# Kernel optimization log

Hardware: AMD Instinct MI355X
Metric: run time of the kernel (lower is better)

## Reference

```python
import jax, jax.numpy as jnp
import numpy as np

N, S, D, E, L = 16, 2048, 256, 512, 4
SEP_P = 1.0 / 48.0  # separator probability -> ~40 ragged subsequences per row


def _ends_per_row(m):
    # Mirrors torch subseqs_from_mask: yields (i, j) for nonempty runs between
    # True separators; we record the LAST index (j-1) of each run.
    ends = []
    i = 0
    Slen = len(m)
    for t in range(Slen):
        if m[t]:
            if i != t:
                ends.append(t - 1)
            i = t + 1
    if i != Slen:
        ends.append(Slen - 1)
    return ends


def _mask_np():
    rng = np.random.default_rng(0)
    return rng.random((N, S)) < SEP_P


def _gather_indices(mask_np):
    ends = [_ends_per_row(row) for row in mask_np]
    Sp = max(max((len(e) for e in ends), default=1), 1)
    idx = np.zeros((len(ends), Sp), dtype=np.int64)
    valid = np.zeros((len(ends), Sp), dtype=bool)
    for i, e in enumerate(ends):
        idx[i, : len(e)] = e
        valid[i, : len(e)] = True
    return idx, valid


def setup_inputs() -> dict:
    key = jax.random.key(0)
    ks = jax.random.split(key, 6)
    k = 1.0 / np.sqrt(E)  # torch LSTM default init scale
    u = lambda kk, shape: jax.random.uniform(kk, shape, jnp.float32, -k, k)
    return {
        "pre_embedding": jax.random.normal(ks[0], (N, S, D), jnp.float32),
        "preembed_mask": jnp.asarray(_mask_np()),
        "W_ih0": u(ks[1], (4 * E, D)),
        "W_ih_rest": u(ks[2], (L - 1, 4 * E, E)),
        "W_hh": u(ks[3], (L, 4 * E, E)),
        "b_ih": u(ks[4], (L, 4 * E)),
        "b_hh": u(ks[5], (L, 4 * E)),
    }


def _lstm_scan(x, sep, W_ih0, W_ih_rest, W_hh, b_ih, b_hh):
    # Fused ragged LSTM: one batched scan over time, resetting (h, c) to zero
    # immediately after separator positions. This reproduces running a fresh
    # LSTM on every mask-delimited subsequence (as the torch loop does).
    # x: (N,S,D), sep: (N,S) bool -> ys: (N,S,E) top-layer outputs.
    n = x.shape[0]
    h0 = jnp.zeros((L, n, E), x.dtype)
    c0 = jnp.zeros((L, n, E), x.dtype)

    def step(carry, inputs):
        h, c = carry
        xt, st = inputs  # (N,D), (N,)
        inp = xt
        hs, cs = [], []
        for l in range(L):
            Wi = W_ih0 if l == 0 else W_ih_rest[l - 1]
            gates = inp @ Wi.T + b_ih[l] + h[l] @ W_hh[l].T + b_hh[l]  # (N,4E)
            gi, gf, gg, go = jnp.split(gates, 4, axis=-1)  # torch gate order i,f,g,o
            cl = jax.nn.sigmoid(gf) * c[l] + jax.nn.sigmoid(gi) * jnp.tanh(gg)
            hl = jax.nn.sigmoid(go) * jnp.tanh(cl)
            hs.append(hl)
            cs.append(cl)
            inp = hl
        h_new = jnp.stack(hs)
        c_new = jnp.stack(cs)
        y = h_new[-1]  # (N,E) top layer output at this step
        reset = st[None, :, None]
        return (jnp.where(reset, 0.0, h_new), jnp.where(reset, 0.0, c_new)), y

    (_, _), ys = jax.lax.scan(step, (h0, c0), (x.transpose(1, 0, 2), sep.T))
    return ys.transpose(1, 0, 2)  # (N,S,E)


def reference(pre_embedding, preembed_mask, W_ih0, W_ih_rest, W_hh, b_ih, b_hh):
    n, s = pre_embedding.shape[:2]
    x = pre_embedding.reshape(n, s, -1)  # Flatten(start_dim=2)
    mask_np = np.asarray(preembed_mask)
    idx, valid = _gather_indices(mask_np)  # (N,Sp) host-side, static structure
    ys = _lstm_scan(x, preembed_mask, W_ih0, W_ih_rest, W_hh, b_ih, b_hh)
    rows = jnp.arange(n)[:, None]
    gathered = ys[rows, jnp.asarray(idx)]  # (N,Sp,E) last output of each subsequence
    valid_j = jnp.asarray(valid)
    ret = jnp.where(valid_j[..., None], gathered, 0.0)  # zero padding as in torch
    out_mask = ~valid_j  # torch returns mask==True for padded slots
    return ret, out_mask
```

## Files before the change

### kernel.cpp

```cpp
#include <hip/hip_runtime.h>
#include <hip/hip_bf16.h>

#define NB 16
#define SB 2048
#define DB 256
#define EB 512
#define LB 4
#define NPAR 4
#define NSEG_CAP 1024
#define GRID_MAIN 128

typedef __bf16 bf16x8 __attribute__((ext_vector_type(8)));
typedef float  f32x4  __attribute__((ext_vector_type(4)));
typedef float  f32x16 __attribute__((ext_vector_type(16)));

#define OFF_XBF   0ull
#define SZ_XBF    (16ull*2048*256*2)
#define OFF_W     (OFF_XBF + SZ_XBF)
#define SZ_W      (4ull*2048*1024*2)
#define OFF_BIAS  (OFF_W + SZ_W)
#define OFF_H     (OFF_BIAS + 4ull*2048*4)
#define SZ_H      (4ull*NPAR*NSEG_CAP*EB*2)
#define OFF_C     (OFF_H + SZ_H)
#define SZ_C      (4ull*NSEG_CAP*EB*4)
#define OFF_SROW   (OFF_C + SZ_C)
#define OFF_SSTART (OFF_SROW  + 4ull*NSEG_CAP)
#define OFF_SLEN   (OFF_SSTART + 4ull*NSEG_CAP)
#define OFF_SSLOT  (OFF_SLEN  + 4ull*NSEG_CAP)
#define OFF_ACT   (OFF_SSLOT + 4ull*NSEG_CAP)
#define OFF_META  (OFF_ACT + 4ull*2048)
#define OFF_FLAGS (OFF_META + 256ull)
#define SZ_FLAGS  (4ull*2048*32*4)

__device__ __forceinline__ unsigned short f2bf(float f) {
  union { float f; unsigned u; } v; v.f = f;
  unsigned r = v.u + 0x7FFFu + ((v.u >> 16) & 1u);
  return (unsigned short)(r >> 16);
}
__device__ __forceinline__ float sigf(float x) {
  x = fminf(30.f, fmaxf(-30.f, x));
  return 1.f / (1.f + __expf(-x));
}
__device__ __forceinline__ float tanhx(float x) {
  x = fminf(15.f, fmaxf(-15.f, x));
  float e = __expf(-2.f * x);
  return (1.f - e) / (1.f + e);
}

__global__ void k_conv(const float* __restrict__ x, const float* __restrict__ wih0,
                       const float* __restrict__ wihr, const float* __restrict__ whh,
                       const float* __restrict__ bih, const float* __restrict__ bhh,
                       float* __restrict__ dout, int out_size, char* __restrict__ ws) {
  long long gid = (long long)blockIdx.x * blockDim.x + threadIdx.x;
  long long stride = (long long)gridDim.x * blockDim.x;
  for (long long i = gid; i < out_size; i += stride) dout[i] = 0.f;
  unsigned* hz = (unsigned*)(ws + OFF_H);
  long long hcw = (long long)(SZ_H + SZ_C) / 4;
  for (long long i = gid; i < hcw; i += stride) hz[i] = 0u;
  unsigned* fz = (unsigned*)(ws + OFF_FLAGS);
  for (long long i = gid; i < (long long)(SZ_FLAGS / 4); i += stride) fz[i] = 0u;
  float* bias = (float*)(ws + OFF_BIAS);
  for (long long i = gid; i < 4 * 2048; i += stride) bias[i] = bih[i] + bhh[i];
  unsigned short* wbf = (unsigned short*)(ws + OFF_W);
  for (long long i = gid; i < 4ll * 2048 * 1024; i += stride) {
    int l = (int)(i >> 21);
    int rem = (int)(i & ((1 << 21) - 1));
    int n = rem >> 10, k = rem & 1023;
    float v;
    if (l == 0)
      v = (k < 256) ? wih0[n * 256 + k]
        : (k < 512) ? 0.f
        : whh[(long long)n * 512 + (k - 512)];
    else
      v = (k < 512) ? wihr[((long long)(l - 1) * 2048 + n) * 512 + k]
                    : whh[((long long)l * 2048 + n) * 512 + (k - 512)];
    wbf[i] = f2bf(v);
  }
  unsigned short* xb = (unsigned short*)(ws + OFF_XBF);
  for (long long i = gid; i < (long long)NB * SB * DB; i += stride) xb[i] = f2bf(x[i]);
}

__global__ void k_seg(const void* __restrict__ maskp, char* __restrict__ ws,
                      float* __restrict__ dout, int Sp) {
  __shared__ unsigned bits[NB][64];
  __shared__ int hist[2050];
  __shared__ int sufx[2051];
  __shared__ int part[256];
  __shared__ unsigned metapk[NSEG_CAP];
  __shared__ int slotar[NSEG_CAP];
  __shared__ int rowcnt[NB];
  __shared__ int flagbits, nseg, maxlen;
  int tid = threadIdx.x;
  if (tid == 0) { flagbits = 0; nseg = 0; maxlen = 0; }
  for (int i = tid; i < 2050; i += 256) hist[i] = 0;
  __syncthreads();
  const unsigned* mw = (const unsigned*)maskp;
  int fb = 0;
  for (int i = tid; i < 8192; i += 256) {
    unsigned w = mw[i];
    if (w == 0x3F800000u) fb |= 2;
    if (w == 0x3FF00000u) fb |= 4;
    if (w & 0xFFFFFF00u) fb |= 1;
    if ((i & 1) && w) fb |= 8;
  }
  if (fb) atomicOr(&flagbits, fb);
  __syncthreads();
  int f = flagbits;
  int kind = (f & 4) ? 3 : (f & 2) ? 2 : (f & 1) ? 0 : (f & 8) ? 1 : 3;
  for (int w = tid; w < NB * 64; w += 256) {
    int row = w >> 6, j = w & 63;
    unsigned b = 0;
    int t0 = j * 32;
    for (int z = 0; z < 32; ++z) {
      long long idx = (long long)row * SB + t0 + z;
      bool sep;
      if (kind == 0)      sep = ((const unsigned char*)maskp)[idx] != 0;
      else if (kind == 1) sep = ((const int*)maskp)[idx] != 0;
      else if (kind == 2) sep = ((const float*)maskp)[idx] != 0.f;
      else                sep = ((const unsigned long long*)maskp)[idx] != 0ull;
      b |= (sep ? 1u : 0u) << z;
    }
    bits[row][j] = b;
  }
  __syncthreads();
  if (tid < NB) {
    int row = tid, i = 0, cnt = 0;
    for (int w = 0; w < 64; ++w) {
      unsigned b = bits[row][w];
      while (b) {
        int z = __ffs(b) - 1; b &= b - 1;
        int t = w * 32 + z;
        if (i != t) {
          int len = t - i;
          int idx = atomicAdd(&nseg, 1);
          if (idx < NSEG_CAP) { metapk[idx] = ((unsigned)row << 23) | ((unsigned)i << 12) | (unsigned)len; slotar[idx] = cnt; }
          atomicAdd(&hist[len], 1); atomicMax(&maxlen, len);
          cnt++;
        }
        i = t + 1;
      }
    }
    if (i != SB) {
      int len = SB - i;
      int idx = atomicAdd(&nseg, 1);
      if (idx < NSEG_CAP) { metapk[idx] = ((unsigned)row << 23) | ((unsigned)i << 12) | (unsigned)len; slotar[idx] = cnt; }
      atomicAdd(&hist[len], 1); atomicMax(&maxlen, len);
      cnt++;
    }
    rowcnt[row] = cnt;
  }
  __syncthreads();
  {
    int lo = tid * 9, hi = lo + 9; if (hi > 2050) hi = 2050;
    int s = 0;
    for (int k = lo; k < hi; ++k) s += hist[k];
    part[tid] = s;
  }
  __syncthreads();
  {
    int tail = 0;
    for (int t2 = tid + 1; t2 < 256; ++t2) tail += part[t2];
    int lo = tid * 9, hi = lo + 9; if (hi > 2050) hi = 2050;
    int run = tail;
    for (int k = hi - 1; k >= lo; --k) { run += hist[k]; sufx[k] = run; }
  }
  __syncthreads();
  int* act = (int*)(ws + OFF_ACT);
  for (int r = tid; r < 2048; r += 256) act[r] = sufx[r + 1];
  for (int i = tid; i < 2050; i += 256) hist[i] = 0;
  __syncthreads();
  int NSEG = nseg < NSEG_CAP ? nseg : NSEG_CAP;
  int* srow = (int*)(ws + OFF_SROW);
  int* sstart = (int*)(ws + OFF_SSTART);
  int* slen = (int*)(ws + OFF_SLEN);
  int* sslot = (int*)(ws + OFF_SSLOT);
  for (int i = tid; i < NSEG; i += 256) {
    unsigned m = metapk[i];
    int len = m & 0xFFF, st = (m >> 12) & 0x7FF, row = (int)(m >> 23);
    int pos = sufx[len + 1] + atomicAdd(&hist[len], 1);
    srow[pos] = row; sstart[pos] = st; slen[pos] = len; sslot[pos] = slotar[i];
  }
  int* meta = (int*)(ws + OFF_META);
  if (tid == 0) { meta[0] = NSEG; meta[1] = maxlen; }
  __syncthreads();
  float* omask = dout + (long long)NB * Sp * EB;
  for (int i = tid; i < NB * Sp; i += 256) {
    int row = i / Sp, slot = i % Sp;
    omask[i] = (slot < rowcnt[row]) ? 0.f : 1.f;
  }
}

__global__ void __launch_bounds__(512, 2)
k_main(char* __restrict__ ws, float* __restrict__ dout, int Sp) {
  __shared__ float glds[2][64][65];
  __shared__ float bias_s[64];
  __shared__ int act_s[2048];
  const int tid = threadIdx.x;
  const int l = blockIdx.x >> 5, wb = blockIdx.x & 31, e0 = wb << 4;
  const int wave = tid >> 6, lane = tid & 63;
  const int mh = wave & 1, kh = (wave >> 1) & 1, rg = wave >> 2;
  const int l31 = lane & 31, lhi = lane >> 5;

  {
    const int* act = (const int*)(ws + OFF_ACT);
    for (int i = tid; i < 2048; i += 512) act_s[i] = act[i];
    if (tid < 64) bias_s[tid] =
        ((const float*)(ws + OFF_BIAS))[l * 2048 + (tid >> 4) * 512 + e0 + (tid & 15)];
  }
  const int maxlen = ((const int*)(ws + OFF_META))[1];
  const char* wsb = ws;

  bf16x8 breg[32];
  {
    int rho = rg * 32 + l31;
    int g = rho >> 4, e = rho & 15;
    const char* wrow = wsb + OFF_W + ((size_t)(l * 2048 + g * 512 + e0 + e)) * 2048;
    const int kbase = kh * 512 + lhi * 8;
    #pragma unroll
    for (int t = 0; t < 32; ++t)
      breg[t] = *(const bf16x8*)(wrow + (size_t)(kbase + t * 16) * 2);
  }
  __syncthreads();

  const int* srow  = (const int*)(ws + OFF_SROW);
  const int* sstart = (const int*)(ws + OFF_SSTART);
  const int* slen  = (const int*)(ws + OFF_SLEN);
  const int* sslot = (const int*)(ws + OFF_SSLOT);
  unsigned* flags = (unsigned*)(ws + OFF_FLAGS);
  const bool l0k0 = (l == 0) && (kh == 0);

  for (int r = 0; r < maxlen; ++r) {
    const bool nA = (l > 0), nB = (r > 0), nC = (l < 3) && (r >= 4);
    if (wave == 0 && (nA | nB | nC)) {
      int li = lane & 31;
      while (true) {
        unsigned ok = 1;
        if (nA) ok &= (__hip_atomic_load(flags + ((((l - 1) * 2048 + r) << 5) + li),
                                         __ATOMIC_RELAXED, __HIP_MEMORY_SCOPE_AGENT) != 0);
        if (nB) ok &= (__hip_atomic_load(flags + (((l * 2048 + (r - 1)) << 5) + li),
                                         __ATOMIC_RELAXED, __HIP_MEMORY_SCOPE_AGENT) != 0);
        if (nC) ok &= (__hip_atomic_load(flags + ((((l + 1) * 2048 + (r - 4)) << 5) + li),
                                         __ATOMIC_RELAXED, __HIP_MEMORY_SCOPE_AGENT) != 0);
        if (__all((int)ok)) break;
        __builtin_amdgcn_s_sleep(2);
      }
      __threadfence();
    }
    __syncthreads();

    const int M = act_s[r];
    const int nmch = (M + 63) >> 6;
    for (int mch = 0; mch < nmch; ++mch) {
      const int segbase = mch << 6;
      int Mv = M - segbase; if (Mv > 64) Mv = 64;
      const int m_l = mh * 32 + l31;
      const int sg = segbase + ((m_l < Mv) ? m_l : 0);
      const char* abase;
      if (kh == 0) {
        if (l == 0) {
          int rw = srow[sg], st = sstart[sg];
          abase = wsb + OFF_XBF + ((size_t)((rw * SB + st + r)) * DB + lhi * 8) * 2;
        } else {
          abase = wsb + OFF_H + ((size_t)((((l - 1) * NPAR + (r & 3)) * NSEG_CAP) + sg) * EB + lhi * 8) * 2;
        }
      } else {
        abase = wsb + OFF_H + ((size_t)(((l * NPAR + ((r - 1) & 3)) * NSEG_CAP) + sg) * EB + lhi * 8) * 2;
      }
      f32x16 acc0 = {0.f}, acc1 = {0.f};
      #pragma unroll
      for (int i = 0; i < 16; ++i) { acc0[i] = 0.f; acc1[i] = 0.f; }
      #pragma unroll
      for (int t = 0; t < 16; t += 2) {
        bf16x8 a0 = *(const bf16x8*)(abase + t * 32);
        acc0 = __builtin_amdgcn_mfma_f32_32x32x16_bf16(a0, breg[t], acc0, 0, 0, 0);
        bf16x8 a1 = *(const bf16x8*)(abase + (t + 1) * 32);
        acc1 = __builtin_amdgcn_mfma_f32_32x32x16_bf16(a1, breg[t + 1], acc1, 0, 0, 0);
      }
      if (!l0k0) {
        #pragma unroll
        for (int t = 16; t < 32; t += 2) {
          bf16x8 a0 = *(const bf16x8*)(abase + t * 32);
          acc0 = __builtin_amdgcn_mfma_f32_32x32x16_bf16(a0, breg[t], acc0, 0, 0, 0);
          bf16x8 a1 = *(const bf16x8*)(abase + (t + 1) * 32);
          acc1 = __builtin_amdgcn_mfma_f32_32x32x16_bf16(a1, breg[t + 1], acc1, 0, 0, 0);
        }
      }
      #pragma unroll
      for (int reg = 0; reg < 16; ++reg) {
        int mm = mh * 32 + (reg & 3) + 8 * (reg >> 2) + 4 * lhi;
        glds[kh][mm][rg * 32 + l31] = acc0[reg] + acc1[reg];
      }
      __syncthreads();
      #pragma unroll
      for (int q = 0; q < 2; ++q) {
        int cell = tid + (q << 9);
        int e = cell & 15, m = cell >> 4;
        if (m < Mv) {
          int sg2 = segbase + m;
          float gi = glds[0][m][e]      + glds[1][m][e]      + bias_s[e];
          float gf = glds[0][m][16 + e] + glds[1][m][16 + e] + bias_s[16 + e];
          float gg = glds[0][m][32 + e] + glds[1][m][32 + e] + bias_s[32 + e];
          float go = glds[0][m][48 + e] + glds[1][m][48 + e] + bias_s[48 + e];
          float* cptr = (float*)(ws + OFF_C + ((size_t)(l * NSEG_CAP + sg2) * EB + e0 + e) * 4);
          float cold = *cptr;
          float cnew = sigf(gf) * cold + sigf(gi) * tanhx(gg);
          float hnew = sigf(go) * tanhx(cnew);
          *cptr = cnew;
          *(unsigned short*)(ws + OFF_H +
              ((size_t)(((l * NPAR + (r & 3)) * NSEG_CAP) + sg2) * EB + e0 + e) * 2) = f2bf(hnew);
          if (l == 3) {
            if (r == slen[sg2] - 1) {
              int rw = srow[sg2], sl = sslot[sg2];
              if (sl < Sp) dout[(((long long)rw * Sp + sl) << 9) + e0 + e] = hnew;
            }
          }
        }
      }
      __syncthreads();
    }
    if (tid == 0) {
      __threadfence();
      __hip_atomic_store(flags + (((l * 2048 + r) << 5) + wb), 1u,
                         __ATOMIC_RELEASE, __HIP_MEMORY_SCOPE_AGENT);
    }
  }
}

extern "C" void kernel_launch(void* const* d_in, const int* in_sizes, int n_in,
                              void* d_out, int out_size, void* d_ws, size_t ws_size,
                              hipStream_t stream) {
  const float* x    = (const float*)d_in[0];
  const void*  mask = d_in[1];
  const float* wih0 = (const float*)d_in[2];
  const float* wihr = (const float*)d_in[3];
  const float* whh  = (const float*)d_in[4];
  const float* bih  = (const float*)d_in[5];
  const float* bhh  = (const float*)d_in[6];
  float* out = (float*)d_out;
  char* ws = (char*)d_ws;
  int Sp = out_size / (NB * (EB + 1));

  k_conv<<<dim3(2048), dim3(256), 0, stream>>>(x, wih0, wihr, whh, bih, bhh, out, out_size, ws);
  k_seg<<<dim3(1), dim3(256), 0, stream>>>(mask, ws, out, Sp);
  k_main<<<dim3(GRID_MAIN), dim3(512), 0, stream>>>(ws, out, Sp);
}
```

Baseline: 7.540 ms.

## Split persistent LSTM wavefront kernel across 512 blocks with LDS-resident weights

The persistent layer-wavefront kernel now uses 128 blocks per layer, each owning 4 hidden units (16 gate rows), instead of 32 blocks of 16 units. Weights move from 32 VGPR bf16x8 registers per lane into an LDS tile, and the matmul switches from 32x32x16 to 16x16x32 MFMA with the K split across two wave groups. Precomputed x offsets and the c-state and segment metadata are prefetched before the MFMA loop. This spreads the per-timestep GEMV across more CUs and lowers register pressure to allow 4 blocks per CU, at the cost of 4x more flag polling per step and more redundant A-operand (h/x) loads across blocks.

```diff
diff --git a/kernel.cpp b/kernel.cpp
--- a/kernel.cpp
+++ b/kernel.cpp
@@ -8,11 +8,10 @@
 #define LB 4
 #define NPAR 4
 #define NSEG_CAP 1024
-#define GRID_MAIN 128
+#define GRID_MAIN 512
 
 typedef __bf16 bf16x8 __attribute__((ext_vector_type(8)));
 typedef float  f32x4  __attribute__((ext_vector_type(4)));
-typedef float  f32x16 __attribute__((ext_vector_type(16)));
 
 #define OFF_XBF   0ull
 #define SZ_XBF    (16ull*2048*256*2)
@@ -27,10 +26,11 @@
 #define OFF_SSTART (OFF_SROW  + 4ull*NSEG_CAP)
 #define OFF_SLEN   (OFF_SSTART + 4ull*NSEG_CAP)
 #define OFF_SSLOT  (OFF_SLEN  + 4ull*NSEG_CAP)
-#define OFF_ACT   (OFF_SSLOT + 4ull*NSEG_CAP)
+#define OFF_XOFF   (OFF_SSLOT + 4ull*NSEG_CAP)
+#define OFF_ACT   (OFF_XOFF + 4ull*NSEG_CAP)
 #define OFF_META  (OFF_ACT + 4ull*2048)
 #define OFF_FLAGS (OFF_META + 256ull)
-#define SZ_FLAGS  (4ull*2048*32*4)
+#define SZ_FLAGS  (4ull*2048*128*4)
 
 __device__ __forceinline__ unsigned short f2bf(float f) {
   union { float f; unsigned u; } v; v.f = f;
@@ -174,11 +174,13 @@
   int* sstart = (int*)(ws + OFF_SSTART);
   int* slen = (int*)(ws + OFF_SLEN);
   int* sslot = (int*)(ws + OFF_SSLOT);
+  int* xoff = (int*)(ws + OFF_XOFF);
   for (int i = tid; i < NSEG; i += 256) {
     unsigned m = metapk[i];
     int len = m & 0xFFF, st = (m >> 12) & 0x7FF, row = (int)(m >> 23);
     int pos = sufx[len + 1] + atomicAdd(&hist[len], 1);
     srow[pos] = row; sstart[pos] = st; slen[pos] = len; sslot[pos] = slotar[i];
+    xoff[pos] = row * SB + st;
   }
   int* meta = (int*)(ws + OFF_META);
   if (tid == 0) { meta[0] = NSEG; meta[1] = maxlen; }
@@ -190,57 +192,57 @@
   }
 }
 
-__global__ void __launch_bounds__(512, 2)
+__global__ void __launch_bounds__(512, 4)
 k_main(char* __restrict__ ws, float* __restrict__ dout, int Sp) {
-  __shared__ float glds[2][64][65];
-  __shared__ float bias_s[64];
-  __shared__ int act_s[2048];
+  __shared__ __align__(16) __bf16 wlds[128][16][8];
+  __shared__ float glds[2][64][17];
+  __shared__ float bias_s[16];
+  __shared__ short act_s[2048];
+  __shared__ unsigned short xoff_s[NSEG_CAP];
   const int tid = threadIdx.x;
-  const int l = blockIdx.x >> 5, wb = blockIdx.x & 31, e0 = wb << 4;
+  const int l = blockIdx.x >> 7, wb = blockIdx.x & 127, e0 = wb << 2;
   const int wave = tid >> 6, lane = tid & 63;
-  const int mh = wave & 1, kh = (wave >> 1) & 1, rg = wave >> 2;
-  const int l31 = lane & 31, lhi = lane >> 5;
+  const int mf = wave & 3, kq = wave >> 2;
+  const int l15 = lane & 15, lq = lane >> 4;
+  const char* wsb = ws;
 
   {
     const int* act = (const int*)(ws + OFF_ACT);
-    for (int i = tid; i < 2048; i += 512) act_s[i] = act[i];
-    if (tid < 64) bias_s[tid] =
-        ((const float*)(ws + OFF_BIAS))[l * 2048 + (tid >> 4) * 512 + e0 + (tid & 15)];
+    for (int i = tid; i < 2048; i += 512) act_s[i] = (short)act[i];
+    const int* xoff = (const int*)(ws + OFF_XOFF);
+    for (int i = tid; i < NSEG_CAP; i += 512) xoff_s[i] = (unsigned short)xoff[i];
+    if (tid < 16) bias_s[tid] =
+        ((const float*)(ws + OFF_BIAS))[l * 2048 + (tid >> 2) * 512 + e0 + (tid & 3)];
+    int rho = tid & 15, g = rho >> 2, e = rho & 3;
+    const unsigned short* wsrc = (const unsigned short*)(wsb + OFF_W)
+        + ((size_t)(l * 2048 + g * 512 + e0 + e)) * 1024;
+    int kg0 = (tid >> 4) * 4;
+    #pragma unroll
+    for (int j = 0; j < 4; ++j)
+      *(bf16x8*)&wlds[kg0 + j][rho][0] = *(const bf16x8*)(wsrc + (size_t)(kg0 + j) * 8);
   }
   const int maxlen = ((const int*)(ws + OFF_META))[1];
-  const char* wsb = ws;
-
-  bf16x8 breg[32];
-  {
-    int rho = rg * 32 + l31;
-    int g = rho >> 4, e = rho & 15;
-    const char* wrow = wsb + OFF_W + ((size_t)(l * 2048 + g * 512 + e0 + e)) * 2048;
-    const int kbase = kh * 512 + lhi * 8;
-    #pragma unroll
-    for (int t = 0; t < 32; ++t)
-      breg[t] = *(const bf16x8*)(wrow + (size_t)(kbase + t * 16) * 2);
-  }
   __syncthreads();
 
   const int* srow  = (const int*)(ws + OFF_SROW);
-  const int* sstart = (const int*)(ws + OFF_SSTART);
   const int* slen  = (const int*)(ws + OFF_SLEN);
   const int* sslot = (const int*)(ws + OFF_SSLOT);
   unsigned* flags = (unsigned*)(ws + OFF_FLAGS);
-  const bool l0k0 = (l == 0) && (kh == 0);
 
   for (int r = 0; r < maxlen; ++r) {
     const bool nA = (l > 0), nB = (r > 0), nC = (l < 3) && (r >= 4);
     if (wave == 0 && (nA | nB | nC)) {
-      int li = lane & 31;
+      const unsigned* pa = flags + ((((l - 1) * 2048 + r) << 7) + lane);
+      const unsigned* pb = flags + (((l * 2048 + (r - 1)) << 7) + lane);
+      const unsigned* pc = flags + ((((l + 1) * 2048 + (r - 4)) << 7) + lane);
       while (true) {
         unsigned ok = 1;
-        if (nA) ok &= (__hip_atomic_load(flags + ((((l - 1) * 2048 + r) << 5) + li),
-                                         __ATOMIC_RELAXED, __HIP_MEMORY_SCOPE_AGENT) != 0);
-        if (nB) ok &= (__hip_atomic_load(flags + (((l * 2048 + (r - 1)) << 5) + li),
-                                         __ATOMIC_RELAXED, __HIP_MEMORY_SCOPE_AGENT) != 0);
-        if (nC) ok &= (__hip_atomic_load(flags + ((((l + 1) * 2048 + (r - 4)) << 5) + li),
-                                         __ATOMIC_RELAXED, __HIP_MEMORY_SCOPE_AGENT) != 0);
+        if (nA) ok &= (__hip_atomic_load(pa, __ATOMIC_RELAXED, __HIP_MEMORY_SCOPE_AGENT) != 0)
+                    & (__hip_atomic_load(pa + 64, __ATOMIC_RELAXED, __HIP_MEMORY_SCOPE_AGENT) != 0);
+        if (nB) ok &= (__hip_atomic_load(pb, __ATOMIC_RELAXED, __HIP_MEMORY_SCOPE_AGENT) != 0)
+                    & (__hip_atomic_load(pb + 64, __ATOMIC_RELAXED, __HIP_MEMORY_SCOPE_AGENT) != 0);
+        if (nC) ok &= (__hip_atomic_load(pc, __ATOMIC_RELAXED, __HIP_MEMORY_SCOPE_AGENT) != 0)
+                    & (__hip_atomic_load(pc + 64, __ATOMIC_RELAXED, __HIP_MEMORY_SCOPE_AGENT) != 0);
         if (__all((int)ok)) break;
         __builtin_amdgcn_s_sleep(2);
       }
@@ -253,74 +255,59 @@
     for (int mch = 0; mch < nmch; ++mch) {
       const int segbase = mch << 6;
       int Mv = M - segbase; if (Mv > 64) Mv = 64;
-      const int m_l = mh * 32 + l31;
+      const int m_l = (mf << 4) + l15;
       const int sg = segbase + ((m_l < Mv) ? m_l : 0);
-      const char* abase;
-      if (kh == 0) {
+      const char* ap;
+      if (kq == 0) {
         if (l == 0) {
-          int rw = srow[sg], st = sstart[sg];
-          abase = wsb + OFF_XBF + ((size_t)((rw * SB + st + r)) * DB + lhi * 8) * 2;
+          ap = wsb + OFF_XBF + (((size_t)((int)xoff_s[sg] + r)) * DB + lq * 8) * 2;
         } else {
-          abase = wsb + OFF_H + ((size_t)((((l - 1) * NPAR + (r & 3)) * NSEG_CAP) + sg) * EB + lhi * 8) * 2;
+          ap = wsb + OFF_H + ((size_t)((((l - 1) * NPAR + (r & 3)) * NSEG_CAP) + sg) * EB + lq * 8) * 2;
         }
       } else {
-        abase = wsb + OFF_H + ((size_t)(((l * NPAR + ((r - 1) & 3)) * NSEG_CAP) + sg) * EB + lhi * 8) * 2;
-      }
-      f32x16 acc0 = {0.f}, acc1 = {0.f};
+        ap = wsb + OFF_H + ((size_t)(((l * NPAR + ((r - 1) & 3)) * NSEG_CAP) + sg) * EB + lq * 8) * 2;
+      }
+      const int em = tid >> 2, ee = tid & 3;
+      float cold = 0.f; int slenv = 0, srowv = 0, sslotv = 0;
+      float* cptr = (float*)(ws + OFF_C + ((size_t)(l * NSEG_CAP + segbase + em) * EB + e0 + ee) * 4);
+      if (tid < 256) {
+        cold = *cptr;
+        if (l == 3) {
+          int sg2 = segbase + em;
+          slenv = slen[sg2]; srowv = srow[sg2]; sslotv = sslot[sg2];
+        }
+      }
+      f32x4 acc = {0.f, 0.f, 0.f, 0.f};
       #pragma unroll
-      for (int i = 0; i < 16; ++i) { acc0[i] = 0.f; acc1[i] = 0.f; }
+      for (int t = 0; t < 16; ++t) {
+        bf16x8 a = *(const bf16x8*)(ap + t * 64);
+        bf16x8 b = *(const bf16x8*)&wlds[(kq << 6) + (t << 2) + lq][l15][0];
+        acc = __builtin_amdgcn_mfma_f32_16x16x32_bf16(a, b, acc, 0, 0, 0);
+      }
       #pragma unroll
-      for (int t = 0; t < 16; t += 2) {
-        bf16x8 a0 = *(const bf16x8*)(abase + t * 32);
-        acc0 = __builtin_amdgcn_mfma_f32_32x32x16_bf16(a0, breg[t], acc0, 0, 0, 0);
-        bf16x8 a1 = *(const bf16x8*)(abase + (t + 1) * 32);
-        acc1 = __builtin_amdgcn_mfma_f32_32x32x16_bf16(a1, breg[t + 1], acc1, 0, 0, 0);
-      }
-      if (!l0k0) {
-        #pragma unroll
-        for (int t = 16; t < 32; t += 2) {
-          bf16x8 a0 = *(const bf16x8*)(abase + t * 32);
-          acc0 = __builtin_amdgcn_mfma_f32_32x32x16_bf16(a0, breg[t], acc0, 0, 0, 0);
-          bf16x8 a1 = *(const bf16x8*)(abase + (t + 1) * 32);
-          acc1 = __builtin_amdgcn_mfma_f32_32x32x16_bf16(a1, breg[t + 1], acc1, 0, 0, 0);
-        }
-      }
-      #pragma unroll
-      for (int reg = 0; reg < 16; ++reg) {
-        int mm = mh * 32 + (reg & 3) + 8 * (reg >> 2) + 4 * lhi;
-        glds[kh][mm][rg * 32 + l31] = acc0[reg] + acc1[reg];
-      }
+      for (int reg = 0; reg < 4; ++reg)
+        glds[kq][(mf << 4) + (lq << 2) + reg][l15] = acc[reg];
       __syncthreads();
-      #pragma unroll
-      for (int q = 0; q < 2; ++q) {
-        int cell = tid + (q << 9);
-        int e = cell & 15, m = cell >> 4;
-        if (m < Mv) {
-          int sg2 = segbase + m;
-          float gi = glds[0][m][e]      + glds[1][m][e]      + bias_s[e];
-          float gf = glds[0][m][16 + e] + glds[1][m][16 + e] + bias_s[16 + e];
-          float gg = glds[0][m][32 + e] + glds[1][m][32 + e] + bias_s[32 + e];
-          float go = glds[0][m][48 + e] + glds[1][m][48 + e] + bias_s[48 + e];
-          float* cptr = (float*)(ws + OFF_C + ((size_t)(l * NSEG_CAP + sg2) * EB + e0 + e) * 4);
-          float cold = *cptr;
-          float cnew = sigf(gf) * cold + sigf(gi) * tanhx(gg);
-          float hnew = sigf(go) * tanhx(cnew);
-          *cptr = cnew;
-          *(unsigned short*)(ws + OFF_H +
-              ((size_t)(((l * NPAR + (r & 3)) * NSEG_CAP) + sg2) * EB + e0 + e) * 2) = f2bf(hnew);
-          if (l == 3) {
-            if (r == slen[sg2] - 1) {
-              int rw = srow[sg2], sl = sslot[sg2];
-              if (sl < Sp) dout[(((long long)rw * Sp + sl) << 9) + e0 + e] = hnew;
-            }
-          }
+      if (tid < 256 && em < Mv) {
+        int sg2 = segbase + em;
+        float gi = glds[0][em][ee]      + glds[1][em][ee]      + bias_s[ee];
+        float gf = glds[0][em][4 + ee]  + glds[1][em][4 + ee]  + bias_s[4 + ee];
+        float gg = glds[0][em][8 + ee]  + glds[1][em][8 + ee]  + bias_s[8 + ee];
+        float go = glds[0][em][12 + ee] + glds[1][em][12 + ee] + bias_s[12 + ee];
+        float cnew = sigf(gf) * cold + sigf(gi) * tanhx(gg);
+        float hnew = sigf(go) * tanhx(cnew);
+        *cptr = cnew;
+        *(unsigned short*)(ws + OFF_H +
+            ((size_t)(((l * NPAR + (r & 3)) * NSEG_CAP) + sg2) * EB + e0 + ee) * 2) = f2bf(hnew);
+        if (l == 3 && r == slenv - 1) {
+          if (sslotv < Sp) dout[(((long long)srowv * Sp + sslotv) << 9) + e0 + ee] = hnew;
         }
       }
       __syncthreads();
     }
     if (tid == 0) {
       __threadfence();
-      __hip_atomic_store(flags + (((l * 2048 + r) << 5) + wb), 1u,
+      __hip_atomic_store(flags + (((l * 2048 + r) << 7) + wb), 1u,
                          __ATOMIC_RELEASE, __HIP_MEMORY_SCOPE_AGENT);
     }
   }
```

After: 15.19 ms. 102% more time.

## Switch recurrent LSTM step to 16x16x32 MFMA tiling with LDS segment metadata

Applied to the files above, without the earlier changes.

Re-tiles the per-step gate GEMM. Each wave now owns one gate (16 columns) across all 64 segments using 16x16x32 bf16 MFMAs, with the K dimension split across two wave groups, instead of 32x32x16 MFMAs over half the rows. Segment metadata (x offsets, lengths, slots, rows) is cached in LDS, the cell state is preloaded before the MFMA loop, and the two K halves are reduced in a single LDS tile. The aim is to cut weight registers, drop global metadata loads from the inner loop, and overlap the c-state load with compute. The trade-off is an extra LDS reduction phase, occupancy lowered to one block per CU, and a larger flags allocation.

```diff
diff --git a/kernel.cpp b/kernel.cpp
--- a/kernel.cpp
+++ b/kernel.cpp
@@ -12,7 +12,6 @@
 
 typedef __bf16 bf16x8 __attribute__((ext_vector_type(8)));
 typedef float  f32x4  __attribute__((ext_vector_type(4)));
-typedef float  f32x16 __attribute__((ext_vector_type(16)));
 
 #define OFF_XBF   0ull
 #define SZ_XBF    (16ull*2048*256*2)
@@ -27,10 +26,11 @@
 #define OFF_SSTART (OFF_SROW  + 4ull*NSEG_CAP)
 #define OFF_SLEN   (OFF_SSTART + 4ull*NSEG_CAP)
 #define OFF_SSLOT  (OFF_SLEN  + 4ull*NSEG_CAP)
-#define OFF_ACT   (OFF_SSLOT + 4ull*NSEG_CAP)
+#define OFF_XOFF   (OFF_SSLOT + 4ull*NSEG_CAP)
+#define OFF_ACT   (OFF_XOFF + 4ull*NSEG_CAP)
 #define OFF_META  (OFF_ACT + 4ull*2048)
 #define OFF_FLAGS (OFF_META + 256ull)
-#define SZ_FLAGS  (4ull*2048*32*4)
+#define SZ_FLAGS  (4ull*2048*128*4)
 
 __device__ __forceinline__ unsigned short f2bf(float f) {
   union { float f; unsigned u; } v; v.f = f;
@@ -174,11 +174,13 @@
   int* sstart = (int*)(ws + OFF_SSTART);
   int* slen = (int*)(ws + OFF_SLEN);
   int* sslot = (int*)(ws + OFF_SSLOT);
+  int* xoff = (int*)(ws + OFF_XOFF);
   for (int i = tid; i < NSEG; i += 256) {
     unsigned m = metapk[i];
     int len = m & 0xFFF, st = (m >> 12) & 0x7FF, row = (int)(m >> 23);
     int pos = sufx[len + 1] + atomicAdd(&hist[len], 1);
     srow[pos] = row; sstart[pos] = st; slen[pos] = len; sslot[pos] = slotar[i];
+    xoff[pos] = row * SB + st;
   }
   int* meta = (int*)(ws + OFF_META);
   if (tid == 0) { meta[0] = NSEG; meta[1] = maxlen; }
@@ -190,44 +192,47 @@
   }
 }
 
-__global__ void __launch_bounds__(512, 2)
+__global__ void __launch_bounds__(512, 1)
 k_main(char* __restrict__ ws, float* __restrict__ dout, int Sp) {
-  __shared__ float glds[2][64][65];
+  __shared__ float glds[64][68];
+  __shared__ unsigned segpk_s[NSEG_CAP];
+  __shared__ unsigned short xoff_s[NSEG_CAP];
+  __shared__ unsigned short act_s[2048];
   __shared__ float bias_s[64];
-  __shared__ int act_s[2048];
   const int tid = threadIdx.x;
   const int l = blockIdx.x >> 5, wb = blockIdx.x & 31, e0 = wb << 4;
   const int wave = tid >> 6, lane = tid & 63;
-  const int mh = wave & 1, kh = (wave >> 1) & 1, rg = wave >> 2;
-  const int l31 = lane & 31, lhi = lane >> 5;
+  const int nq = wave & 3, kh = wave >> 2;
+  const int l15 = lane & 15, lq = lane >> 4;
+  const char* wsb = ws;
 
   {
     const int* act = (const int*)(ws + OFF_ACT);
-    for (int i = tid; i < 2048; i += 512) act_s[i] = act[i];
+    for (int i = tid; i < 2048; i += 512) act_s[i] = (unsigned short)act[i];
+    const int* xoff = (const int*)(ws + OFF_XOFF);
+    const int* srow = (const int*)(ws + OFF_SROW);
+    const int* slen = (const int*)(ws + OFF_SLEN);
+    const int* sslot = (const int*)(ws + OFF_SSLOT);
+    for (int i = tid; i < NSEG_CAP; i += 512) {
+      xoff_s[i] = (unsigned short)xoff[i];
+      segpk_s[i] = ((unsigned)slen[i] & 0xFFFu) | (((unsigned)sslot[i] & 0xFFFu) << 16)
+                 | (((unsigned)srow[i] & 0xFu) << 28);
+    }
     if (tid < 64) bias_s[tid] =
         ((const float*)(ws + OFF_BIAS))[l * 2048 + (tid >> 4) * 512 + e0 + (tid & 15)];
   }
   const int maxlen = ((const int*)(ws + OFF_META))[1];
-  const char* wsb = ws;
-
-  bf16x8 breg[32];
+
+  bf16x8 breg[16];
   {
-    int rho = rg * 32 + l31;
-    int g = rho >> 4, e = rho & 15;
-    const char* wrow = wsb + OFF_W + ((size_t)(l * 2048 + g * 512 + e0 + e)) * 2048;
-    const int kbase = kh * 512 + lhi * 8;
+    const char* wrow = wsb + OFF_W + ((size_t)(l * 2048 + nq * 512 + e0 + l15)) * 2048;
     #pragma unroll
-    for (int t = 0; t < 32; ++t)
-      breg[t] = *(const bf16x8*)(wrow + (size_t)(kbase + t * 16) * 2);
-  }
-  __syncthreads();
-
-  const int* srow  = (const int*)(ws + OFF_SROW);
-  const int* sstart = (const int*)(ws + OFF_SSTART);
-  const int* slen  = (const int*)(ws + OFF_SLEN);
-  const int* sslot = (const int*)(ws + OFF_SSLOT);
+    for (int t = 0; t < 16; ++t)
+      breg[t] = *(const bf16x8*)(wrow + (size_t)(kh * 512 + t * 32 + lq * 8) * 2);
+  }
+  __syncthreads();
+
   unsigned* flags = (unsigned*)(ws + OFF_FLAGS);
-  const bool l0k0 = (l == 0) && (kh == 0);
 
   for (int r = 0; r < maxlen; ++r) {
     const bool nA = (l > 0), nB = (r > 0), nC = (l < 3) && (r >= 4);
@@ -253,65 +258,74 @@
     for (int mch = 0; mch < nmch; ++mch) {
       const int segbase = mch << 6;
       int Mv = M - segbase; if (Mv > 64) Mv = 64;
-      const int m_l = mh * 32 + l31;
-      const int sg = segbase + ((m_l < Mv) ? m_l : 0);
-      const char* abase;
+      const char* ap[4];
+      #pragma unroll
+      for (int mf = 0; mf < 4; ++mf) {
+        int m_l = (mf << 4) + l15;
+        int sg = segbase + ((m_l < Mv) ? m_l : 0);
+        const char* base;
+        if (kh == 0) {
+          if (l == 0)
+            base = wsb + OFF_XBF + (((size_t)((int)xoff_s[sg] + r)) * DB) * 2;
+          else
+            base = wsb + OFF_H + ((size_t)((((l - 1) * NPAR + (r & 3)) * NSEG_CAP) + sg) * EB) * 2;
+        } else {
+          base = wsb + OFF_H + ((size_t)(((l * NPAR + ((r - 1) & 3)) * NSEG_CAP) + sg) * EB) * 2;
+        }
+        ap[mf] = base + lq * 16;
+      }
+      const int em = tid >> 4, ee = tid & 15;
+      float* cp0 = (float*)(ws + OFF_C + ((size_t)(l * NSEG_CAP + segbase + em) * EB + e0 + ee) * 4);
+      float* cp1 = (float*)(ws + OFF_C + ((size_t)(l * NSEG_CAP + segbase + em + 32) * EB + e0 + ee) * 4);
+      float cold0 = *cp0, cold1 = *cp1;
+      f32x4 acc[4];
+      #pragma unroll
+      for (int mf = 0; mf < 4; ++mf) acc[mf] = (f32x4){0.f, 0.f, 0.f, 0.f};
+      #pragma unroll
+      for (int t = 0; t < 16; ++t) {
+        #pragma unroll
+        for (int mf = 0; mf < 4; ++mf) {
+          bf16x8 a = *(const bf16x8*)(ap[mf] + t * 64);
+          acc[mf] = __builtin_amdgcn_mfma_f32_16x16x32_bf16(a, breg[t], acc[mf], 0, 0, 0);
+        }
+      }
       if (kh == 0) {
-        if (l == 0) {
-          int rw = srow[sg], st = sstart[sg];
-          abase = wsb + OFF_XBF + ((size_t)((rw * SB + st + r)) * DB + lhi * 8) * 2;
-        } else {
-          abase = wsb + OFF_H + ((size_t)((((l - 1) * NPAR + (r & 3)) * NSEG_CAP) + sg) * EB + lhi * 8) * 2;
-        }
-      } else {
-        abase = wsb + OFF_H + ((size_t)(((l * NPAR + ((r - 1) & 3)) * NSEG_CAP) + sg) * EB + lhi * 8) * 2;
-      }
-      f32x16 acc0 = {0.f}, acc1 = {0.f};
-      #pragma unroll
-      for (int i = 0; i < 16; ++i) { acc0[i] = 0.f; acc1[i] = 0.f; }
-      #pragma unroll
-      for (int t = 0; t < 16; t += 2) {
-        bf16x8 a0 = *(const bf16x8*)(abase + t * 32);
-        acc0 = __builtin_amdgcn_mfma_f32_32x32x16_bf16(a0, breg[t], acc0, 0, 0, 0);
-        bf16x8 a1 = *(const bf16x8*)(abase + (t + 1) * 32);
-        acc1 = __builtin_amdgcn_mfma_f32_32x32x16_bf16(a1, breg[t + 1], acc1, 0, 0, 0);
-      }
-      if (!l0k0) {
         #pragma unroll
-        for (int t = 16; t < 32; t += 2) {
-          bf16x8 a0 = *(const bf16x8*)(abase + t * 32);
-          acc0 = __builtin_amdgcn_mfma_f32_32x32x16_bf16(a0, breg[t], acc0, 0, 0, 0);
-          bf16x8 a1 = *(const bf16x8*)(abase + (t + 1) * 32);
-          acc1 = __builtin_amdgcn_mfma_f32_32x32x16_bf16(a1, breg[t + 1], acc1, 0, 0, 0);
-        }
-      }
-      #pragma unroll
-      for (int reg = 0; reg < 16; ++reg) {
-        int mm = mh * 32 + (reg & 3) + 8 * (reg >> 2) + 4 * lhi;
-        glds[kh][mm][rg * 32 + l31] = acc0[reg] + acc1[reg];
+        for (int mf = 0; mf < 4; ++mf)
+          #pragma unroll
+          for (int reg = 0; reg < 4; ++reg)
+            glds[(mf << 4) + (lq << 2) + reg][(nq << 4) + l15] = acc[mf][reg];
+      }
+      __syncthreads();
+      if (kh == 1) {
+        #pragma unroll
+        for (int mf = 0; mf < 4; ++mf)
+          #pragma unroll
+          for (int reg = 0; reg < 4; ++reg)
+            glds[(mf << 4) + (lq << 2) + reg][(nq << 4) + l15] += acc[mf][reg];
       }
       __syncthreads();
       #pragma unroll
       for (int q = 0; q < 2; ++q) {
-        int cell = tid + (q << 9);
-        int e = cell & 15, m = cell >> 4;
+        int m = em + (q << 5);
+        float cold = q ? cold1 : cold0;
+        float* cptr = q ? cp1 : cp0;
         if (m < Mv) {
           int sg2 = segbase + m;
-          float gi = glds[0][m][e]      + glds[1][m][e]      + bias_s[e];
-          float gf = glds[0][m][16 + e] + glds[1][m][16 + e] + bias_s[16 + e];
-          float gg = glds[0][m][32 + e] + glds[1][m][32 + e] + bias_s[32 + e];
-          float go = glds[0][m][48 + e] + glds[1][m][48 + e] + bias_s[48 + e];
-          float* cptr = (float*)(ws + OFF_C + ((size_t)(l * NSEG_CAP + sg2) * EB + e0 + e) * 4);
-          float cold = *cptr;
+          float gi = glds[m][ee]      + bias_s[ee];
+          float gf = glds[m][16 + ee] + bias_s[16 + ee];
+          float gg = glds[m][32 + ee] + bias_s[32 + ee];
+          float go = glds[m][48 + ee] + bias_s[48 + ee];
           float cnew = sigf(gf) * cold + sigf(gi) * tanhx(gg);
           float hnew = sigf(go) * tanhx(cnew);
           *cptr = cnew;
           *(unsigned short*)(ws + OFF_H +
-              ((size_t)(((l * NPAR + (r & 3)) * NSEG_CAP) + sg2) * EB + e0 + e) * 2) = f2bf(hnew);
+              ((size_t)(((l * NPAR + (r & 3)) * NSEG_CAP) + sg2) * EB + e0 + ee) * 2) = f2bf(hnew);
           if (l == 3) {
-            if (r == slen[sg2] - 1) {
-              int rw = srow[sg2], sl = sslot[sg2];
-              if (sl < Sp) dout[(((long long)rw * Sp + sl) << 9) + e0 + e] = hnew;
+            unsigned pk = segpk_s[sg2];
+            if (r == (int)(pk & 0xFFFu) - 1) {
+              int sl = (int)((pk >> 16) & 0xFFFu), rw = (int)(pk >> 28);
+              if (sl < Sp) dout[(((long long)rw * Sp + sl) << 9) + e0 + ee] = hnew;
             }
           }
         }
```

Result: slower. 10.94 ms (+45.1%).
